# Kernel tuning notes

Measured on AMD Instinct MI355X. Metric: run time of the kernel, lower is better.

## Reference

```python
import jax, jax.numpy as jnp
import numpy as np

N_NODES = 50000


def _gcn_conv(x, src, dst, W, b, n):
    # PyG GCNConv: h = x @ W; symmetric normalization with self-loops; scatter-add; + bias
    h = x @ W
    deg = jax.ops.segment_sum(jnp.ones_like(dst, dtype=h.dtype), dst, num_segments=n)
    dinv = jax.lax.rsqrt(jnp.maximum(deg, 1.0))  # self-loops guarantee deg >= 1
    norm = dinv[src] * dinv[dst]                 # [E_total]
    msgs = h[src] * norm[:, None]                # gather + scale
    out = jax.ops.segment_sum(msgs, dst, num_segments=n)
    return out + b


def setup_inputs() -> dict:
    key = jax.random.key(0)
    k1, k2, k3, k4 = jax.random.split(key, 4)
    d, f = 128, 128
    x = jax.random.normal(k1, (N_NODES, d), dtype=jnp.float32)
    edge_index = jax.random.randint(k2, (2, 800000), 0, N_NODES, dtype=jnp.int64)
    W1 = jax.random.normal(k3, (d, f), dtype=jnp.float32) / np.sqrt(d)
    b1 = jnp.zeros((f,), dtype=jnp.float32)
    W2 = jax.random.normal(k4, (f, 1), dtype=jnp.float32) / np.sqrt(f)
    b2 = jnp.zeros((1,), dtype=jnp.float32)
    return {"x": x, "edge_index": edge_index, "W1": W1, "b1": b1, "W2": W2, "b2": b2}


def reference(x, edge_index, W1, b1, W2, b2):
    n = x.shape[0]
    loops = jnp.arange(n, dtype=edge_index.dtype)
    src = jnp.concatenate([edge_index[0], loops])
    dst = jnp.concatenate([edge_index[1], loops])
    h = _gcn_conv(x, src, dst, W1, b1, n)
    h = jax.nn.relu(h)
    out = _gcn_conv(h, src, dst, W2, b2, n)
    return out
```

## Files before the change

### kernel.cpp

```cpp
#include <hip/hip_runtime.h>
#include <hip/hip_fp16.h>

#define D 128
#define BINW 128
#define BINCAP 4096
#define SUBT 1568

typedef _Float16 half8 __attribute__((ext_vector_type(8)));
typedef float float4v __attribute__((ext_vector_type(4)));

__global__ __launch_bounds__(256) void fused_bin_gemm_kernel(
    const float* __restrict__ x, const float* __restrict__ W,
    __half* __restrict__ h, const int* __restrict__ idx,
    int* __restrict__ binCount, unsigned* __restrict__ binned,
    int E, int nbin, int n, int SB) {
  __shared__ uint4 smem[2048];
  const int t = threadIdx.x;

  if (blockIdx.x < SB) {
    int*            hist  = (int*)smem;
    int*            cur   = hist + 512;
    unsigned*       recs  = (unsigned*)(cur + 512);
    unsigned short* dbins = (unsigned short*)(recs + SUBT);
    int*            isp   = (int*)(dbins + SUBT);

    for (int b = t; b < 512; b += 256) hist[b] = 0;
    if (t == 0) {
      int any = 0;
      for (int i = 0; i < 64; ++i) any |= idx[2 * i + 1];
      *isp = (any == 0) ? 1 : 0;
    }
    __syncthreads();
    const int is64 = *isp;
    const int lo = blockIdx.x * SUBT;
    const int hi = min(lo + SUBT, E);
    const int cnt = hi - lo;

    for (int e = lo + t; e < hi; e += 256) {
      int s, d;
      if (is64) { s = idx[2 * e]; d = idx[2 * (E + e)]; }
      else      { s = idx[e];     d = idx[E + e]; }
      const int li = e - lo;
      const int b = d >> 7;
      recs[li]  = (unsigned)s | ((unsigned)(d & 127) << 16);
      dbins[li] = (unsigned short)b;
      atomicAdd(&hist[b], 1);
    }
    __syncthreads();
    for (int b = t; b < nbin; b += 256) {
      int hv = hist[b];
      cur[b] = hv ? atomicAdd(&binCount[b], hv) : 0;
    }
    __syncthreads();
    for (int li = t; li < cnt; li += 256) {
      const int b = dbins[li];
      int pos = atomicAdd(&cur[b], 1);
      pos = min(pos, BINCAP - 1);
      binned[(size_t)b * BINCAP + pos] = recs[li];
    }
  } else {
    const int bid = blockIdx.x - SB;
    uint4 (*bfrag)[4][64] = (uint4(*)[4][64])smem;

    for (int e = t; e < 2048; e += 256) {
      const int nt = e >> 8;
      const int kk = (e >> 6) & 3;
      const int L  = e & 63;
      const int nn = nt * 16 + (L & 15);
      const int k0 = kk * 32 + (L >> 4) * 8;
      half8 v;
#pragma unroll
      for (int j = 0; j < 8; ++j) v[j] = (_Float16)W[(k0 + j) * D + nn];
      bfrag[nt][kk][L] = *(uint4*)&v;
    }
    __syncthreads();

    const int wave = t >> 6;
    const int lane = t & 63;
    const int r0 = bid * 64 + wave * 16;

    const int mrow = r0 + (lane & 15);
    const int mc = (mrow < n) ? mrow : (n - 1);
    half8 af[4];
#pragma unroll
    for (int kk = 0; kk < 4; ++kk) {
      const float* xp = x + (size_t)mc * D + kk * 32 + (lane >> 4) * 8;
      float4 lo4 = *(const float4*)xp;
      float4 hi4 = *(const float4*)(xp + 4);
      half8 v;
      v[0] = (_Float16)lo4.x; v[1] = (_Float16)lo4.y;
      v[2] = (_Float16)lo4.z; v[3] = (_Float16)lo4.w;
      v[4] = (_Float16)hi4.x; v[5] = (_Float16)hi4.y;
      v[6] = (_Float16)hi4.z; v[7] = (_Float16)hi4.w;
      af[kk] = v;
    }

    float4v acc[8];
#pragma unroll
    for (int nt = 0; nt < 8; ++nt) acc[nt] = (float4v){0.f, 0.f, 0.f, 0.f};

#pragma unroll
    for (int nt = 0; nt < 8; ++nt) {
      uint4 b0 = bfrag[nt][0][lane];
      uint4 b1 = bfrag[nt][1][lane];
      uint4 b2 = bfrag[nt][2][lane];
      uint4 b3 = bfrag[nt][3][lane];
      acc[nt] = __builtin_amdgcn_mfma_f32_16x16x32_f16(af[0], *(half8*)&b0, acc[nt], 0, 0, 0);
      acc[nt] = __builtin_amdgcn_mfma_f32_16x16x32_f16(af[1], *(half8*)&b1, acc[nt], 0, 0, 0);
      acc[nt] = __builtin_amdgcn_mfma_f32_16x16x32_f16(af[2], *(half8*)&b2, acc[nt], 0, 0, 0);
      acc[nt] = __builtin_amdgcn_mfma_f32_16x16x32_f16(af[3], *(half8*)&b3, acc[nt], 0, 0, 0);
    }

    __syncthreads();
    __half* hout = (__half*)smem;
    const int quad = lane >> 4;
    const int col  = lane & 15;
    const int rloc = wave * 16 + quad * 4;
#pragma unroll
    for (int r = 0; r < 4; ++r)
#pragma unroll
      for (int nt = 0; nt < 8; ++nt)
        hout[(rloc + r) * D + nt * 16 + col] = __float2half(acc[nt][r]);
    __syncthreads();

    const size_t rowbase = (size_t)bid * 64;
#pragma unroll
    for (int i = 0; i < 4; ++i) {
      const int elt = i * 256 + t;
      const int rr  = elt >> 4;
      if (rowbase + rr < (size_t)n)
        *(uint4*)(h + (rowbase + rr) * D + (elt & 15) * 8) = smem[elt];
    }
  }
}

__global__ __launch_bounds__(256) void bin_sort_kernel(const int* __restrict__ binCount,
                                                       const unsigned* __restrict__ binned,
                                                       unsigned short* __restrict__ csr,
                                                       int* __restrict__ rowptr,
                                                       int* __restrict__ rend,
                                                       float* __restrict__ dinv,
                                                       int n, int nbin) {
  __shared__ unsigned rec[BINCAP];
  __shared__ unsigned short srt[BINCAP];
  __shared__ int hist[BINW];
  __shared__ int scn[BINW];
  __shared__ int cur[BINW];
  const int t = threadIdx.x;
  const int b = blockIdx.x;
  int cnt = binCount[b];
  if (cnt > BINCAP) cnt = BINCAP;
  const size_t gbase = (size_t)b * BINCAP;

  for (int i = t; i < cnt; i += 256) rec[i] = binned[gbase + i];
  if (t < BINW) hist[t] = 0;
  __syncthreads();
  for (int i = t; i < cnt; i += 256) atomicAdd(&hist[rec[i] >> 16], 1);
  __syncthreads();
  if (t < BINW) scn[t] = hist[t];
  __syncthreads();
  for (int off = 1; off < BINW; off <<= 1) {
    int u = 0;
    if (t < BINW && t >= off) u = scn[t - off];
    __syncthreads();
    if (t < BINW) scn[t] += u;
    __syncthreads();
  }
  if (t < BINW) cur[t] = scn[t] - hist[t];
  __syncthreads();
  for (int i = t; i < cnt; i += 256) {
    unsigned r = rec[i];
    int pos = atomicAdd(&cur[r >> 16], 1);
    srt[pos] = (unsigned short)(r & 0xFFFFu);
  }
  __syncthreads();
  const unsigned* srt32 = (const unsigned*)srt;
  unsigned* csr32 = (unsigned*)(csr + gbase);
  for (int i = t; i < (cnt + 1) / 2; i += 256) csr32[i] = srt32[i];

  const int node = b * BINW + t;
  if (t < BINW && node < n) {
    int deg = hist[t];
    int start = (int)gbase + (scn[t] - deg);
    rowptr[node] = start;
    rend[node]   = start + deg;
    dinv[node]   = rsqrtf((float)(deg + 1));
  }
}

__device__ __forceinline__ void unpack8(uint4 p, float f[8]) {
  float2 t;
  t = __half22float2(*(__half2*)&p.x); f[0] = t.x; f[1] = t.y;
  t = __half22float2(*(__half2*)&p.y); f[2] = t.x; f[3] = t.y;
  t = __half22float2(*(__half2*)&p.z); f[4] = t.x; f[5] = t.y;
  t = __half22float2(*(__half2*)&p.w); f[6] = t.x; f[7] = t.y;
}

__global__ __launch_bounds__(256) void gather1_kernel(const __half* __restrict__ h,
                                                      const int* __restrict__ rowptr,
                                                      const int* __restrict__ rend,
                                                      const unsigned short* __restrict__ csr,
                                                      const float* __restrict__ dinv,
                                                      const float* __restrict__ b1,
                                                      const float* __restrict__ W2,
                                                      float* __restrict__ zw, int n) {
  const int node = blockIdx.x * 4 + (threadIdx.x >> 6);
  if (node >= n) return;
  const int lane = threadIdx.x & 63;
  const int q    = lane >> 4;
  const int fb   = (lane & 15) * 8;

  const float di = dinv[node];
  float a[8] = {0.f, 0.f, 0.f, 0.f, 0.f, 0.f, 0.f, 0.f};
  if (q == 0) {
    uint4 p = *(const uint4*)(h + (size_t)node * D + fb);
    float f[8]; unpack8(p, f);
    float s2 = di * di;
#pragma unroll
    for (int k = 0; k < 8; ++k) a[k] = f[k] * s2;
  }

  const int end = rend[node];
  for (int j = rowptr[node] + q; j < end; j += 16) {
    const int j1 = j + 4, j2 = j + 8, j3 = j + 12;
    const bool v1 = j1 < end, v2 = j2 < end, v3 = j3 < end;
    int s0 = csr[j];
    int s1 = v1 ? csr[j1] : s0;
    int s2 = v2 ? csr[j2] : s0;
    int s3 = v3 ? csr[j3] : s0;
    uint4 p0 = *(const uint4*)(h + (size_t)s0 * D + fb);
    uint4 p1 = *(const uint4*)(h + (size_t)s1 * D + fb);
    uint4 p2 = *(const uint4*)(h + (size_t)s2 * D + fb);
    uint4 p3 = *(const uint4*)(h + (size_t)s3 * D + fb);
    float w0 = di * dinv[s0];
    float w1 = v1 ? di * dinv[s1] : 0.f;
    float w2 = v2 ? di * dinv[s2] : 0.f;
    float w3 = v3 ? di * dinv[s3] : 0.f;
    float f0[8], f1[8], f2[8], f3[8];
    unpack8(p0, f0); unpack8(p1, f1); unpack8(p2, f2); unpack8(p3, f3);
#pragma unroll
    for (int k = 0; k < 8; ++k) a[k] = fmaf(f0[k], w0, a[k]);
#pragma unroll
    for (int k = 0; k < 8; ++k) a[k] = fmaf(f1[k], w1, a[k]);
#pragma unroll
    for (int k = 0; k < 8; ++k) a[k] = fmaf(f2[k], w2, a[k]);
#pragma unroll
    for (int k = 0; k < 8; ++k) a[k] = fmaf(f3[k], w3, a[k]);
  }

#pragma unroll
  for (int k = 0; k < 8; ++k) {
    a[k] += __shfl_xor(a[k], 16, 64);
    a[k] += __shfl_xor(a[k], 32, 64);
  }

  float4 blo = *(const float4*)(b1 + fb);
  float4 bhi = *(const float4*)(b1 + fb + 4);
  float4 wlo = *(const float4*)(W2 + fb);
  float4 whi = *(const float4*)(W2 + fb + 4);
  float bb[8] = {blo.x, blo.y, blo.z, blo.w, bhi.x, bhi.y, bhi.z, bhi.w};
  float ww[8] = {wlo.x, wlo.y, wlo.z, wlo.w, whi.x, whi.y, whi.z, whi.w};
  float p = 0.f;
#pragma unroll
  for (int k = 0; k < 8; ++k) p += fmaxf(a[k] + bb[k], 0.f) * ww[k];
#pragma unroll
  for (int off = 8; off > 0; off >>= 1) p += __shfl_xor(p, off, 64);
  if (lane == 0) zw[node] = p * di;
}

__global__ void gather2_kernel(const float* __restrict__ zw,
                               const float* __restrict__ dinv,
                               const int* __restrict__ rowptr,
                               const int* __restrict__ rend,
                               const unsigned short* __restrict__ csr,
                               const float* __restrict__ b2,
                               float* __restrict__ out, int n) {
  int i = blockIdx.x * blockDim.x + threadIdx.x;
  if (i >= n) return;
  float s = zw[i];
  const int lo = rowptr[i], hi = rend[i];
  int j = lo;
  for (; j + 4 <= hi; j += 4) {
    int a0 = csr[j], a1 = csr[j + 1], a2 = csr[j + 2], a3 = csr[j + 3];
    s += zw[a0] + zw[a1] + zw[a2] + zw[a3];
  }
  for (; j < hi; ++j) s += zw[csr[j]];
  out[i] = s * dinv[i] + b2[0];
}

extern "C" void kernel_launch(void* const* d_in, const int* in_sizes, int n_in,
                              void* d_out, int out_size, void* d_ws, size_t ws_size,
                              hipStream_t stream) {
  const float* x   = (const float*)d_in[0];
  const int*   idx = (const int*)d_in[1];
  const float* W1  = (const float*)d_in[2];
  const float* b1  = (const float*)d_in[3];
  const float* W2  = (const float*)d_in[4];
  const float* b2  = (const float*)d_in[5];
  float* out = (float*)d_out;

  const int n = in_sizes[0] / D;
  const int E = in_sizes[1] / 2;
  const int nbin = (n + BINW - 1) / BINW;

  char* ws = (char*)d_ws;
  size_t off = 0;
  auto carve = [&](size_t bytes) { char* p = ws + off; off += (bytes + 255) & ~(size_t)255; return p; };
  int*            binCount = (int*)carve((size_t)nbin * 4);
  unsigned*       binned   = (unsigned*)carve((size_t)nbin * BINCAP * 4);
  unsigned short* csr      = (unsigned short*)carve((size_t)nbin * BINCAP * 2);
  int*            rowptr   = (int*)carve((size_t)n * 4);
  int*            rend     = (int*)carve((size_t)n * 4);
  float*          dinv     = (float*)carve((size_t)n * 4);
  __half*         h        = (__half*)carve((size_t)n * D * 2);
  float*          zw       = (float*)carve((size_t)n * 4);

  const int SB = (E + SUBT - 1) / SUBT;
  const int GB = (n + 63) / 64;

  hipMemsetAsync(binCount, 0, (size_t)nbin * 4, stream);
  fused_bin_gemm_kernel<<<SB + GB, 256, 0, stream>>>(x, W1, h, idx, binCount,
                                                     binned, E, nbin, n, SB);
  bin_sort_kernel<<<nbin, 256, 0, stream>>>(binCount, binned, csr, rowptr, rend, dinv, n, nbin);
  gather1_kernel<<<(n + 3) / 4, 256, 0, stream>>>(h, rowptr, rend, csr, dinv, b1, W2, zw, n);
  gather2_kernel<<<(n + 255) / 256, 256, 0, stream>>>(zw, dinv, rowptr, rend, csr, b2, out, n);
}
```

Measured before the change: 157.2 us.

## Replace bin-sort CSR build with per-node atomic adjacency lists

```diff
diff --git a/kernel.cpp b/kernel.cpp
--- a/kernel.cpp
+++ b/kernel.cpp
@@ -2,29 +2,22 @@
 #include <hip/hip_fp16.h>
 
 #define D 128
-#define BINW 128
-#define BINCAP 4096
-#define SUBT 1568
+#define LCAP 64
+#define SUBT 3136
 
 typedef _Float16 half8 __attribute__((ext_vector_type(8)));
 typedef float float4v __attribute__((ext_vector_type(4)));
 
-__global__ __launch_bounds__(256) void fused_bin_gemm_kernel(
+__global__ __launch_bounds__(256) void fused_scatter_gemm_kernel(
     const float* __restrict__ x, const float* __restrict__ W,
     __half* __restrict__ h, const int* __restrict__ idx,
-    int* __restrict__ binCount, unsigned* __restrict__ binned,
-    int E, int nbin, int n, int SB) {
+    int* __restrict__ cnt, unsigned short* __restrict__ lists,
+    int E, int n, int SB) {
   __shared__ uint4 smem[2048];
   const int t = threadIdx.x;
 
   if (blockIdx.x < SB) {
-    int*            hist  = (int*)smem;
-    int*            cur   = hist + 512;
-    unsigned*       recs  = (unsigned*)(cur + 512);
-    unsigned short* dbins = (unsigned short*)(recs + SUBT);
-    int*            isp   = (int*)(dbins + SUBT);
-
-    for (int b = t; b < 512; b += 256) hist[b] = 0;
+    int* isp = (int*)smem;
     if (t == 0) {
       int any = 0;
       for (int i = 0; i < 64; ++i) any |= idx[2 * i + 1];
@@ -34,29 +27,21 @@
     const int is64 = *isp;
     const int lo = blockIdx.x * SUBT;
     const int hi = min(lo + SUBT, E);
-    const int cnt = hi - lo;
-
-    for (int e = lo + t; e < hi; e += 256) {
-      int s, d;
-      if (is64) { s = idx[2 * e]; d = idx[2 * (E + e)]; }
-      else      { s = idx[e];     d = idx[E + e]; }
-      const int li = e - lo;
-      const int b = d >> 7;
-      recs[li]  = (unsigned)s | ((unsigned)(d & 127) << 16);
-      dbins[li] = (unsigned short)b;
-      atomicAdd(&hist[b], 1);
-    }
-    __syncthreads();
-    for (int b = t; b < nbin; b += 256) {
-      int hv = hist[b];
-      cur[b] = hv ? atomicAdd(&binCount[b], hv) : 0;
-    }
-    __syncthreads();
-    for (int li = t; li < cnt; li += 256) {
-      const int b = dbins[li];
-      int pos = atomicAdd(&cur[b], 1);
-      pos = min(pos, BINCAP - 1);
-      binned[(size_t)b * BINCAP + pos] = recs[li];
+    if (is64) {
+      const int2* p = (const int2*)idx;
+      for (int e = lo + t; e < hi; e += 256) {
+        const int s = p[e].x;
+        const int d = p[E + e].x;
+        const int pos = atomicAdd(&cnt[d], 1);
+        if (pos < LCAP) lists[(size_t)d * LCAP + pos] = (unsigned short)s;
+      }
+    } else {
+      for (int e = lo + t; e < hi; e += 256) {
+        const int s = idx[e];
+        const int d = idx[E + e];
+        const int pos = atomicAdd(&cnt[d], 1);
+        if (pos < LCAP) lists[(size_t)d * LCAP + pos] = (unsigned short)s;
+      }
     }
   } else {
     const int bid = blockIdx.x - SB;
@@ -134,60 +119,6 @@
   }
 }
 
-__global__ __launch_bounds__(256) void bin_sort_kernel(const int* __restrict__ binCount,
-                                                       const unsigned* __restrict__ binned,
-                                                       unsigned short* __restrict__ csr,
-                                                       int* __restrict__ rowptr,
-                                                       int* __restrict__ rend,
-                                                       float* __restrict__ dinv,
-                                                       int n, int nbin) {
-  __shared__ unsigned rec[BINCAP];
-  __shared__ unsigned short srt[BINCAP];
-  __shared__ int hist[BINW];
-  __shared__ int scn[BINW];
-  __shared__ int cur[BINW];
-  const int t = threadIdx.x;
-  const int b = blockIdx.x;
-  int cnt = binCount[b];
-  if (cnt > BINCAP) cnt = BINCAP;
-  const size_t gbase = (size_t)b * BINCAP;
-
-  for (int i = t; i < cnt; i += 256) rec[i] = binned[gbase + i];
-  if (t < BINW) hist[t] = 0;
-  __syncthreads();
-  for (int i = t; i < cnt; i += 256) atomicAdd(&hist[rec[i] >> 16], 1);
-  __syncthreads();
-  if (t < BINW) scn[t] = hist[t];
-  __syncthreads();
-  for (int off = 1; off < BINW; off <<= 1) {
-    int u = 0;
-    if (t < BINW && t >= off) u = scn[t - off];
-    __syncthreads();
-    if (t < BINW) scn[t] += u;
-    __syncthreads();
-  }
-  if (t < BINW) cur[t] = scn[t] - hist[t];
-  __syncthreads();
-  for (int i = t; i < cnt; i += 256) {
-    unsigned r = rec[i];
-    int pos = atomicAdd(&cur[r >> 16], 1);
-    srt[pos] = (unsigned short)(r & 0xFFFFu);
-  }
-  __syncthreads();
-  const unsigned* srt32 = (const unsigned*)srt;
-  unsigned* csr32 = (unsigned*)(csr + gbase);
-  for (int i = t; i < (cnt + 1) / 2; i += 256) csr32[i] = srt32[i];
-
-  const int node = b * BINW + t;
-  if (t < BINW && node < n) {
-    int deg = hist[t];
-    int start = (int)gbase + (scn[t] - deg);
-    rowptr[node] = start;
-    rend[node]   = start + deg;
-    dinv[node]   = rsqrtf((float)(deg + 1));
-  }
-}
-
 __device__ __forceinline__ void unpack8(uint4 p, float f[8]) {
   float2 t;
   t = __half22float2(*(__half2*)&p.x); f[0] = t.x; f[1] = t.y;
@@ -197,10 +128,8 @@
 }
 
 __global__ __launch_bounds__(256) void gather1_kernel(const __half* __restrict__ h,
-                                                      const int* __restrict__ rowptr,
-                                                      const int* __restrict__ rend,
-                                                      const unsigned short* __restrict__ csr,
-                                                      const float* __restrict__ dinv,
+                                                      const int* __restrict__ cnt,
+                                                      const unsigned short* __restrict__ lists,
                                                       const float* __restrict__ b1,
                                                       const float* __restrict__ W2,
                                                       float* __restrict__ zw, int n) {
@@ -210,7 +139,9 @@
   const int q    = lane >> 4;
   const int fb   = (lane & 15) * 8;
 
-  const float di = dinv[node];
+  const int  c   = cnt[node];
+  const int  deg = min(c, LCAP);
+  const float di = rsqrtf((float)(c + 1));
   float a[8] = {0.f, 0.f, 0.f, 0.f, 0.f, 0.f, 0.f, 0.f};
   if (q == 0) {
     uint4 p = *(const uint4*)(h + (size_t)node * D + fb);
@@ -220,22 +151,22 @@
     for (int k = 0; k < 8; ++k) a[k] = f[k] * s2;
   }
 
-  const int end = rend[node];
-  for (int j = rowptr[node] + q; j < end; j += 16) {
+  const unsigned short* lst = lists + (size_t)node * LCAP;
+  for (int j = q; j < deg; j += 16) {
     const int j1 = j + 4, j2 = j + 8, j3 = j + 12;
-    const bool v1 = j1 < end, v2 = j2 < end, v3 = j3 < end;
-    int s0 = csr[j];
-    int s1 = v1 ? csr[j1] : s0;
-    int s2 = v2 ? csr[j2] : s0;
-    int s3 = v3 ? csr[j3] : s0;
+    const bool v1 = j1 < deg, v2 = j2 < deg, v3 = j3 < deg;
+    int s0 = lst[j];
+    int s1 = v1 ? lst[j1] : s0;
+    int s2 = v2 ? lst[j2] : s0;
+    int s3 = v3 ? lst[j3] : s0;
     uint4 p0 = *(const uint4*)(h + (size_t)s0 * D + fb);
     uint4 p1 = *(const uint4*)(h + (size_t)s1 * D + fb);
     uint4 p2 = *(const uint4*)(h + (size_t)s2 * D + fb);
     uint4 p3 = *(const uint4*)(h + (size_t)s3 * D + fb);
-    float w0 = di * dinv[s0];
-    float w1 = v1 ? di * dinv[s1] : 0.f;
-    float w2 = v2 ? di * dinv[s2] : 0.f;
-    float w3 = v3 ? di * dinv[s3] : 0.f;
+    float w0 = di * rsqrtf((float)(cnt[s0] + 1));
+    float w1 = v1 ? di * rsqrtf((float)(cnt[s1] + 1)) : 0.f;
+    float w2 = v2 ? di * rsqrtf((float)(cnt[s2] + 1)) : 0.f;
+    float w3 = v3 ? di * rsqrtf((float)(cnt[s3] + 1)) : 0.f;
     float f0[8], f1[8], f2[8], f3[8];
     unpack8(p0, f0); unpack8(p1, f1); unpack8(p2, f2); unpack8(p3, f3);
 #pragma unroll
@@ -268,24 +199,22 @@
   if (lane == 0) zw[node] = p * di;
 }
 
-__global__ void gather2_kernel(const float* __restrict__ zw,
-                               const float* __restrict__ dinv,
-                               const int* __restrict__ rowptr,
-                               const int* __restrict__ rend,
-                               const unsigned short* __restrict__ csr,
-                               const float* __restrict__ b2,
-                               float* __restrict__ out, int n) {
-  int i = blockIdx.x * blockDim.x + threadIdx.x;
-  if (i >= n) return;
-  float s = zw[i];
-  const int lo = rowptr[i], hi = rend[i];
-  int j = lo;
-  for (; j + 4 <= hi; j += 4) {
-    int a0 = csr[j], a1 = csr[j + 1], a2 = csr[j + 2], a3 = csr[j + 3];
-    s += zw[a0] + zw[a1] + zw[a2] + zw[a3];
-  }
-  for (; j < hi; ++j) s += zw[csr[j]];
-  out[i] = s * dinv[i] + b2[0];
+__global__ __launch_bounds__(256) void gather2_kernel(const float* __restrict__ zw,
+                                                      const int* __restrict__ cnt,
+                                                      const unsigned short* __restrict__ lists,
+                                                      const float* __restrict__ b2,
+                                                      float* __restrict__ out, int n) {
+  const int node = blockIdx.x * 64 + (threadIdx.x >> 2);
+  if (node >= n) return;
+  const int l = threadIdx.x & 3;
+  const int c = cnt[node];
+  const int deg = min(c, LCAP);
+  const unsigned short* lst = lists + (size_t)node * LCAP;
+  float s = (l == 0) ? zw[node] : 0.f;
+  for (int j = l; j < deg; j += 4) s += zw[lst[j]];
+  s += __shfl_xor(s, 1, 64);
+  s += __shfl_xor(s, 2, 64);
+  if (l == 0) out[node] = s * rsqrtf((float)(c + 1)) + b2[0];
 }
 
 extern "C" void kernel_launch(void* const* d_in, const int* in_sizes, int n_in,
@@ -301,27 +230,20 @@
 
   const int n = in_sizes[0] / D;
   const int E = in_sizes[1] / 2;
-  const int nbin = (n + BINW - 1) / BINW;
 
   char* ws = (char*)d_ws;
   size_t off = 0;
   auto carve = [&](size_t bytes) { char* p = ws + off; off += (bytes + 255) & ~(size_t)255; return p; };
-  int*            binCount = (int*)carve((size_t)nbin * 4);
-  unsigned*       binned   = (unsigned*)carve((size_t)nbin * BINCAP * 4);
-  unsigned short* csr      = (unsigned short*)carve((size_t)nbin * BINCAP * 2);
-  int*            rowptr   = (int*)carve((size_t)n * 4);
-  int*            rend     = (int*)carve((size_t)n * 4);
-  float*          dinv     = (float*)carve((size_t)n * 4);
-  __half*         h        = (__half*)carve((size_t)n * D * 2);
-  float*          zw       = (float*)carve((size_t)n * 4);
+  int*            cnt   = (int*)carve((size_t)n * 4);
+  unsigned short* lists = (unsigned short*)carve((size_t)n * LCAP * 2);
+  __half*         h     = (__half*)carve((size_t)n * D * 2);
+  float*          zw    = (float*)carve((size_t)n * 4);
 
   const int SB = (E + SUBT - 1) / SUBT;
   const int GB = (n + 63) / 64;
 
-  hipMemsetAsync(binCount, 0, (size_t)nbin * 4, stream);
-  fused_bin_gemm_kernel<<<SB + GB, 256, 0, stream>>>(x, W1, h, idx, binCount,
-                                                     binned, E, nbin, n, SB);
-  bin_sort_kernel<<<nbin, 256, 0, stream>>>(binCount, binned, csr, rowptr, rend, dinv, n, nbin);
-  gather1_kernel<<<(n + 3) / 4, 256, 0, stream>>>(h, rowptr, rend, csr, dinv, b1, W2, zw, n);
-  gather2_kernel<<<(n + 255) / 256, 256, 0, stream>>>(zw, dinv, rowptr, rend, csr, b2, out, n);
-}
+  hipMemsetAsync(cnt, 0, (size_t)n * 4, stream);
+  fused_scatter_gemm_kernel<<<SB + GB, 256, 0, stream>>>(x, W1, h, idx, cnt, lists, E, n, SB);
+  gather1_kernel<<<(n + 3) / 4, 256, 0, stream>>>(h, cnt, lists, b1, W2, zw, n);
+  gather2_kernel<<<(n + 63) / 64, 256, 0, stream>>>(zw, cnt, lists, b2, out, n);
+}
```

Result: slower. 170.0 us (+8.1%).
